# Performance work log

Hardware: AMD Instinct MI355X
Metric: run time of the kernel (lower is better)

## Reference

```python
import jax, jax.numpy as jnp
import numpy as np
from jax import lax

IMG = 512
STRIDE = 32
FH = IMG // STRIDE  # 16
TOP_N = 1000
NCLS = 6  # num_classes + background
BBOX_CLAMP = float(np.log(1000.0 / 16.0))


def _conv(x, w, b, stride, pad):
    y = lax.conv_general_dilated(x, w, (stride, stride), [(pad, pad), (pad, pad)],
                                 dimension_numbers=('NCHW', 'OIHW', 'NCHW'))
    return y + b[None, :, None, None]


def _decode(deltas, boxes, weights):
    # torchvision BoxCoder.decode_single; deltas (N,K,4), boxes (N,4) xyxy
    wx, wy, ww, wh = weights
    widths = boxes[:, 2] - boxes[:, 0]
    heights = boxes[:, 3] - boxes[:, 1]
    cx = boxes[:, 0] + 0.5 * widths
    cy = boxes[:, 1] + 0.5 * heights
    dx = deltas[..., 0] / wx
    dy = deltas[..., 1] / wy
    dw = jnp.minimum(deltas[..., 2] / ww, BBOX_CLAMP)
    dh = jnp.minimum(deltas[..., 3] / wh, BBOX_CLAMP)
    pcx = dx * widths[:, None] + cx[:, None]
    pcy = dy * heights[:, None] + cy[:, None]
    pw = jnp.exp(dw) * widths[:, None]
    ph = jnp.exp(dh) * heights[:, None]
    return jnp.stack([pcx - 0.5 * pw, pcy - 0.5 * ph,
                      pcx + 0.5 * pw, pcy + 0.5 * ph], axis=-1)


def _anchors():
    # AnchorGenerator(sizes=(128,256,512), ratios=(0.5,1,2)), single stride-32 level
    scales = np.array([128.0, 256.0, 512.0])
    ratios = np.array([0.5, 1.0, 2.0])
    h_r = np.sqrt(ratios)
    w_r = 1.0 / h_r
    ws = (w_r[:, None] * scales[None, :]).reshape(-1)
    hs = (h_r[:, None] * scales[None, :]).reshape(-1)
    cell = np.round(np.stack([-ws, -hs, ws, hs], axis=1) / 2.0)  # (9,4)
    sy, sx = np.meshgrid(np.arange(FH) * STRIDE, np.arange(FH) * STRIDE, indexing='ij')
    shifts = np.stack([sx.reshape(-1), sy.reshape(-1), sx.reshape(-1), sy.reshape(-1)], axis=1)
    anc = (shifts[:, None, :] + cell[None, :, :]).reshape(-1, 4)  # (FH*FH*9, 4), (h,w,A) order
    return jnp.asarray(anc, jnp.float32)


def _roi_align(feat_nhwc, rois, bidx):
    # torchvision roi_align: output 7x7, sampling_ratio=2, spatial_scale=1/32, aligned=False
    scale = 1.0 / STRIDE
    Wf = feat_nhwc.shape[1]
    x1 = rois[:, 0] * scale
    y1 = rois[:, 1] * scale
    x2 = rois[:, 2] * scale
    y2 = rois[:, 3] * scale
    rw = jnp.maximum(x2 - x1, 1.0)
    rh = jnp.maximum(y2 - y1, 1.0)
    # 14 = 7 bins * 2 samples; point k sits at (k+0.5)*bin/2 from roi start
    g = (jnp.arange(14, dtype=jnp.float32) + 0.5) / 14.0
    px = jnp.clip(x1[:, None] + g[None, :] * rw[:, None], 0.0, Wf - 1)  # (R,14)
    py = jnp.clip(y1[:, None] + g[None, :] * rh[:, None], 0.0, Wf - 1)
    x0 = jnp.floor(px).astype(jnp.int32)
    y0 = jnp.floor(py).astype(jnp.int32)
    x1i = jnp.minimum(x0 + 1, Wf - 1)
    y1i = jnp.minimum(y0 + 1, Wf - 1)
    lx = px - x0.astype(px.dtype)
    ly = py - y0.astype(py.dtype)
    hx = 1.0 - lx
    hy = 1.0 - ly
    b = bidx[:, None, None]

    def gat(yi, xi):
        return feat_nhwc[b, yi[:, :, None], xi[:, None, :]]  # (R,14,14,C)

    ly_ = ly[:, :, None, None]; hy_ = hy[:, :, None, None]
    lx_ = lx[:, None, :, None]; hx_ = hx[:, None, :, None]
    s = (hy_ * hx_ * gat(y0, x0) + hy_ * lx_ * gat(y0, x1i)
         + ly_ * hx_ * gat(y1i, x0) + ly_ * lx_ * gat(y1i, x1i))  # (R,14,14,C)
    R, C = s.shape[0], s.shape[3]
    pooled = s.reshape(R, 7, 2, 7, 2, C).mean(axis=(2, 4))  # (R,7,7,C)
    return pooled.transpose(0, 3, 1, 2).reshape(R, C * 49)


def _forward(images, c0_w, c0_b, c1_w, c1_b, c2_w, c2_b, c3_w, c3_b,
             rpn_conv_w, rpn_conv_b, rpn_cls_w, rpn_cls_b, rpn_bbox_w, rpn_bbox_b,
             fc1_w, fc1_b, fc2_w, fc2_b, cls_w, cls_b, bbox_w, bbox_b):
    B = images.shape[0]
    # GeneralizedRCNNTransform: normalize; resize is identity (512 == min_size)
    mean = jnp.array([0.485, 0.456, 0.406], jnp.float32).reshape(1, 3, 1, 1)
    std = jnp.array([0.229, 0.224, 0.225], jnp.float32).reshape(1, 3, 1, 1)
    x = (images - mean) / std
    # backbone: stride-32, 512-channel feature extractor (resnet34-style features_only)
    x = jax.nn.relu(_conv(x, c0_w, c0_b, 2, 3))
    x = lax.reduce_window(x, -jnp.inf, lax.max, (1, 1, 3, 3), (1, 1, 2, 2),
                          [(0, 0), (0, 0), (1, 1), (1, 1)])
    x = jax.nn.relu(_conv(x, c1_w, c1_b, 2, 1))
    x = jax.nn.relu(_conv(x, c2_w, c2_b, 2, 1))
    feat = jax.nn.relu(_conv(x, c3_w, c3_b, 2, 1))  # (B,512,16,16)
    # RPN head
    t = jax.nn.relu(_conv(feat, rpn_conv_w, rpn_conv_b, 1, 1))
    obj = _conv(t, rpn_cls_w, rpn_cls_b, 1, 0)   # (B,9,16,16)
    bd = _conv(t, rpn_bbox_w, rpn_bbox_b, 1, 0)  # (B,36,16,16)
    _, A, H, W = obj.shape
    # concat_box_prediction_layers ordering: (H,W,A)
    obj_f = lax.stop_gradient(obj.transpose(0, 2, 3, 1).reshape(B, -1))  # (B,N)
    bd_f = lax.stop_gradient(
        bd.reshape(B, A, 4, H, W).transpose(0, 3, 4, 1, 2).reshape(B, -1, 4))  # (B,N,4)
    anchors = _anchors()  # (N,4)
    props = _decode(bd_f.transpose(1, 0, 2), anchors, (1.0, 1.0, 1.0, 1.0)).transpose(1, 0, 2)
    # _get_top_n_idx (single level, eval pre_nms_top_n=1000) + gather + clip
    _, top_idx = lax.top_k(obj_f, TOP_N)
    props = props[jnp.arange(B)[:, None], top_idx]  # (B,TOP_N,4)
    props = jnp.clip(props, 0.0, float(IMG))
    rois = props.reshape(-1, 4)
    bidx = jnp.repeat(jnp.arange(B), TOP_N)
    # MultiScaleRoIAlign -> TwoMLPHead -> FastRCNNPredictor
    bf = _roi_align(feat.transpose(0, 2, 3, 1), rois, bidx)  # (R, 512*49)
    h = jax.nn.relu(bf @ fc1_w + fc1_b)
    h = jax.nn.relu(h @ fc2_w + fc2_b)
    logits = h @ cls_w + cls_b  # (R,6)
    breg = h @ bbox_w + bbox_b  # (R,24)
    pred = _decode(breg.reshape(-1, NCLS, 4), rois, (10.0, 10.0, 5.0, 5.0))  # (R,6,4)
    scores = jax.nn.softmax(logits, axis=1)[:, 1:]   # drop background -> (R,5)
    boxes = jnp.clip(pred, 0.0, float(IMG))[:, 1:]   # (R,5,4)
    # resize ratios original/transformed = 512/512 = 1.0 -> coordinate rescale is identity
    out = jnp.concatenate([boxes, scores[:, :, None]], axis=2)  # (R,5,5)
    return out.reshape(B, -1, NCLS - 1, 5)  # (B,1000,5,5)


_SHAPES = {
    'c0_w': (64, 3, 7, 7), 'c0_b': (64,),
    'c1_w': (128, 64, 3, 3), 'c1_b': (128,),
    'c2_w': (256, 128, 3, 3), 'c2_b': (256,),
    'c3_w': (512, 256, 3, 3), 'c3_b': (512,),
    'rpn_conv_w': (512, 512, 3, 3), 'rpn_conv_b': (512,),
    'rpn_cls_w': (9, 512, 1, 1), 'rpn_cls_b': (9,),
    'rpn_bbox_w': (36, 512, 1, 1), 'rpn_bbox_b': (36,),
    'fc1_w': (25088, 1024), 'fc1_b': (1024,),
    'fc2_w': (1024, 1024), 'fc2_b': (1024,),
    'cls_w': (1024, 6), 'cls_b': (6,),
    'bbox_w': (1024, 24), 'bbox_b': (24,),
}


def setup_inputs() -> dict:
    key = jax.random.key(0)
    ks = jax.random.split(key, len(_SHAPES) + 1)
    inp = {'images': jax.random.normal(ks[0], (1, 3, IMG, IMG), jnp.float32)}
    for i, (name, shp) in enumerate(_SHAPES.items()):
        if name.endswith('_b'):
            inp[name] = jnp.zeros(shp, jnp.float32)
        else:
            fan_in = int(np.prod(shp[1:])) if len(shp) == 4 else int(shp[0])
            scale = float(np.sqrt(2.0 / fan_in))
            if name in ('rpn_bbox_w', 'bbox_w'):
                scale *= 0.1  # keep box deltas small/realistic
            inp[name] = jax.random.normal(ks[i + 1], shp, jnp.float32) * scale
    return inp


def reference(images, c0_w, c0_b, c1_w, c1_b, c2_w, c2_b, c3_w, c3_b,
              rpn_conv_w, rpn_conv_b, rpn_cls_w, rpn_cls_b, rpn_bbox_w, rpn_bbox_b,
              fc1_w, fc1_b, fc2_w, fc2_b, cls_w, cls_b, bbox_w, bbox_b):
    return _forward(images, c0_w, c0_b, c1_w, c1_b, c2_w, c2_b, c3_w, c3_b,
                    rpn_conv_w, rpn_conv_b, rpn_cls_w, rpn_cls_b, rpn_bbox_w, rpn_bbox_b,
                    fc1_w, fc1_b, fc2_w, fc2_b, cls_w, cls_b, bbox_w, bbox_b)
```

## Files before the change

kernel.cpp:

```cpp
#include <hip/hip_runtime.h>
#include <cstdint>
#include <cstddef>


typedef float  f4  __attribute__((ext_vector_type(4)));
typedef short  s8v __attribute__((ext_vector_type(8)));

__device__ __forceinline__ unsigned short f2bf(float f) {
  unsigned int u = __builtin_bit_cast(unsigned int, f);
  u += 0x7FFFu + ((u >> 16) & 1u);
  return (unsigned short)(u >> 16);
}
__device__ __forceinline__ float bf2f(unsigned short h) {
  unsigned int u = ((unsigned int)h) << 16;
  return __builtin_bit_cast(float, u);
}

#define BBOX_CLAMP_F 4.135166556742356f

__global__ __launch_bounds__(256, 2) void conv0_kernel(
    const float* __restrict__ img, const float* __restrict__ w,
    const float* __restrict__ bias, float* __restrict__ out) {
  __shared__ float patch[3][37][40];
  __shared__ float wlds[32][3][7][8];
  const int tid = threadIdx.x;
  const int tx0 = blockIdx.x * 16, ty0 = blockIdx.y * 16;
  const int ocb = blockIdx.z * 32;
  for (int idx = tid; idx < 3 * 37 * 40; idx += 256) {
    int c = idx / 1480; int rem = idx - c * 1480; int r = rem / 40; int col = rem - r * 40;
    float v = 0.f;
    int iy = ty0 * 2 - 3 + r, ix = tx0 * 2 - 3 + col;
    if (col < 37 && iy >= 0 && iy < 512 && ix >= 0 && ix < 512) {
      float mval = (c == 0) ? 0.485f : (c == 1) ? 0.456f : 0.406f;
      float sval = (c == 0) ? 0.229f : (c == 1) ? 0.224f : 0.225f;
      v = (img[c * 262144 + iy * 512 + ix] - mval) / sval;
    }
    (&patch[0][0][0])[idx] = v;
  }
  for (int idx = tid; idx < 32 * 3 * 7 * 8; idx += 256) {
    int oc = idx / 168; int rem = idx - oc * 168; int c = rem / 56;
    int rem2 = rem - c * 56; int ky = rem2 >> 3; int kx = rem2 & 7;
    (&wlds[0][0][0][0])[idx] = (kx < 7) ? w[(ocb + oc) * 147 + c * 49 + ky * 7 + kx] : 0.f;
  }
  __syncthreads();
  const int ocg = tid >> 5, cell = tid & 31;
  const int cx = cell & 3, cy = cell >> 2;
  float acc[4][2][4] = {};
  for (int c = 0; c < 3; ++c) {
    for (int ky = 0; ky < 7; ++ky) {
      const float* p0 = &patch[c][cy * 4 + ky][cx * 8];
      const float* p1 = &patch[c][cy * 4 + ky + 2][cx * 8];
      f4 a0[4], a1[4];
      #pragma unroll
      for (int q = 0; q < 4; ++q) { a0[q] = *(const f4*)(p0 + q * 4); a1[q] = *(const f4*)(p1 + q * 4); }
      #pragma unroll
      for (int oc = 0; oc < 4; ++oc) {
        const float* wp = &wlds[ocg * 4 + oc][c][ky][0];
        f4 w0 = *(const f4*)wp, w1 = *(const f4*)(wp + 4);
        #pragma unroll
        for (int kx = 0; kx < 7; ++kx) {
          float wv = (kx < 4) ? w0[kx] : w1[kx - 4];
          #pragma unroll
          for (int x = 0; x < 4; ++x) {
            int e = x * 2 + kx;
            acc[oc][0][x] += a0[e >> 2][e & 3] * wv;
            acc[oc][1][x] += a1[e >> 2][e & 3] * wv;
          }
        }
      }
    }
  }
  #pragma unroll
  for (int oc = 0; oc < 4; ++oc) {
    float b = bias[ocb + ocg * 4 + oc];
    #pragma unroll
    for (int r = 0; r < 2; ++r) {
      f4 v;
      #pragma unroll
      for (int x = 0; x < 4; ++x) v[x] = fmaxf(acc[oc][r][x] + b, 0.f);
      *(f4*)&out[(size_t)(ocb + ocg * 4 + oc) * 65536 + (size_t)(ty0 + cy * 2 + r) * 256 + tx0 + cx * 4] = v;
    }
  }
}

__global__ __launch_bounds__(256) void maxpool_kernel(
    const float* __restrict__ in, float* __restrict__ out) {
  int i = blockIdx.x * 256 + threadIdx.x;
  int c = i >> 14; int y = (i >> 7) & 127; int x = i & 127;
  float m = -INFINITY;
  #pragma unroll
  for (int dy = 0; dy < 3; ++dy) {
    int yy = 2 * y - 1 + dy;
    if (yy < 0 || yy >= 256) continue;
    #pragma unroll
    for (int dx = 0; dx < 3; ++dx) {
      int xx = 2 * x - 1 + dx;
      if (xx < 0 || xx >= 256) continue;
      m = fmaxf(m, in[c * 65536 + yy * 256 + xx]);
    }
  }
  out[i] = m;
}

template<int CIN, int COUT, int HIN, int HOUT, int STR, int TILES_X, int CSPL>
__global__ __launch_bounds__(256, 2) void conv3x3_kernel(
    const float* __restrict__ in, const float* __restrict__ w,
    float* __restrict__ parts) {
  constexpr int TW = 16, TH = 16;
  constexpr int SPAN  = (TH - 1) * STR + 3;
  constexpr int SPANW = (TW - 1) * STR + 3;
  constexpr int PADW  = (SPANW + 3) & ~3;
  __shared__ float patch[8][SPAN][PADW];
  __shared__ float wlds[32][8][3][4];
  const int tid = threadIdx.x;
  const int tile = blockIdx.x;
  const int tx0 = (tile % TILES_X) * TW, ty0 = (tile / TILES_X) * TH;
  const int ocb = blockIdx.y * 32;
  const int cb0 = blockIdx.z * CSPL;
  const int ocg = tid >> 5, cell = tid & 31;
  const int cx = cell & 3, cy = cell >> 2;
  float acc[4][2][4] = {};
  for (int cc = 0; cc < CSPL / 8; ++cc) {
    int cbase = cb0 + cc * 8;
    __syncthreads();
    for (int idx = tid; idx < 8 * SPAN * PADW; idx += 256) {
      int ch = idx / (SPAN * PADW);
      int rem = idx - ch * (SPAN * PADW);
      int r = rem / PADW;
      int col = rem - r * PADW;
      float v = 0.f;
      int iy = ty0 * STR - 1 + r, ix = tx0 * STR - 1 + col;
      if (col < SPANW && iy >= 0 && iy < HIN && ix >= 0 && ix < HIN)
        v = in[(size_t)(cbase + ch) * (HIN * HIN) + iy * HIN + ix];
      (&patch[0][0][0])[idx] = v;
    }
    for (int idx = tid; idx < 32 * 8 * 3 * 4; idx += 256) {
      int oc = idx / 96;
      int rem = idx - oc * 96;
      int ch = rem / 12;
      int rem2 = rem - ch * 12;
      int ky = rem2 >> 2, kx = rem2 & 3;
      (&wlds[0][0][0][0])[idx] = (kx < 3)
        ? w[((size_t)(ocb + oc) * CIN + cbase + ch) * 9 + ky * 3 + kx] : 0.f;
    }
    __syncthreads();
    #pragma unroll 1
    for (int ch = 0; ch < 8; ++ch) {
      #pragma unroll
      for (int ky = 0; ky < 3; ++ky) {
        constexpr int NF = (STR == 2) ? 3 : 2;
        const float* p0 = &patch[ch][(cy * 2 + 0) * STR + ky][cx * 4 * STR];
        const float* p1 = &patch[ch][(cy * 2 + 1) * STR + ky][cx * 4 * STR];
        f4 a0[NF], a1[NF];
        #pragma unroll
        for (int q = 0; q < NF; ++q) { a0[q] = *(const f4*)(p0 + q * 4); a1[q] = *(const f4*)(p1 + q * 4); }
        #pragma unroll
        for (int oc = 0; oc < 4; ++oc) {
          f4 wv = *(const f4*)&wlds[ocg * 4 + oc][ch][ky][0];
          #pragma unroll
          for (int kx = 0; kx < 3; ++kx) {
            #pragma unroll
            for (int x = 0; x < 4; ++x) {
              int e = x * STR + kx;
              acc[oc][0][x] += a0[e >> 2][e & 3] * wv[kx];
              acc[oc][1][x] += a1[e >> 2][e & 3] * wv[kx];
            }
          }
        }
      }
    }
  }
  size_t zb = (size_t)blockIdx.z * COUT * HOUT * HOUT;
  #pragma unroll
  for (int oc = 0; oc < 4; ++oc) {
    #pragma unroll
    for (int r = 0; r < 2; ++r) {
      f4 v;
      #pragma unroll
      for (int x = 0; x < 4; ++x) v[x] = acc[oc][r][x];
      *(f4*)&parts[zb + (size_t)(ocb + ocg * 4 + oc) * (HOUT * HOUT)
                   + (size_t)(ty0 + cy * 2 + r) * HOUT + tx0 + cx * 4] = v;
    }
  }
}

template<int NS>
__global__ __launch_bounds__(256) void reduce_conv_kernel(
    const float* __restrict__ parts, const float* __restrict__ bias,
    float* __restrict__ out, int total4, int hwshift,
    unsigned short* __restrict__ nhwc, float* __restrict__ nhwc32, int C) {
  int i4 = blockIdx.x * 256 + threadIdx.x;
  if (i4 >= total4) return;
  const f4* p4 = (const f4*)parts;
  f4 s = {0.f, 0.f, 0.f, 0.f};
  #pragma unroll
  for (int k = 0; k < NS; ++k) s += p4[(size_t)k * total4 + i4];
  int i = i4 * 4;
  int c = i >> hwshift;
  float b = bias[c];
  #pragma unroll
  for (int j = 0; j < 4; ++j) s[j] = fmaxf(s[j] + b, 0.f);
  ((f4*)out)[i4] = s;
  int hw = 1 << hwshift;
  int px = i & (hw - 1);
  if (nhwc) {
    #pragma unroll
    for (int j = 0; j < 4; ++j) nhwc[(size_t)(px + j) * C + c] = f2bf(s[j]);
  }
  if (nhwc32) {
    #pragma unroll
    for (int j = 0; j < 4; ++j) nhwc32[(size_t)(px + j) * C + c] = s[j];
  }
}

__global__ __launch_bounds__(64) void rpn_head_kernel(
    const float* __restrict__ tn, const float* __restrict__ wc,
    const float* __restrict__ bc, const float* __restrict__ wb,
    const float* __restrict__ bb, float* __restrict__ objf,
    float* __restrict__ bdf) {
  int px = blockIdx.x, lane = threadIdx.x;
  float acc[45] = {};
  for (int j = 0; j < 8; ++j) {
    int c = j * 64 + lane;
    float tv = tn[px * 512 + c];
    #pragma unroll
    for (int a = 0; a < 9; ++a) acc[a] += tv * wc[a * 512 + c];
    #pragma unroll
    for (int o = 0; o < 36; ++o) acc[9 + o] += tv * wb[o * 512 + c];
  }
  #pragma unroll
  for (int o = 0; o < 45; ++o) {
    #pragma unroll
    for (int m = 32; m; m >>= 1) acc[o] += __shfl_xor(acc[o], m);
  }
  if (lane == 0) {
    #pragma unroll
    for (int a = 0; a < 9; ++a) objf[px * 9 + a] = acc[a] + bc[a];
    #pragma unroll
    for (int a = 0; a < 9; ++a)
      #pragma unroll
      for (int q = 0; q < 4; ++q)
        bdf[(px * 9 + a) * 4 + q] = acc[9 + a * 4 + q] + bb[a * 4 + q];
  }
}

__device__ const float g_W2[9] = {91.f, 181.f, 362.f, 64.f, 128.f, 256.f, 45.f, 91.f, 181.f};
__device__ const float g_H2[9] = {45.f, 91.f, 181.f, 64.f, 128.f, 256.f, 91.f, 181.f, 362.f};

__global__ __launch_bounds__(256) void props_kernel(
    const float* __restrict__ bdf, float* __restrict__ props) {
  int i = blockIdx.x * 256 + threadIdx.x;
  if (i >= 2304) return;
  int pix = i / 9; int a = i - pix * 9;
  int y = pix >> 4, x = pix & 15;
  float wid = 2.f * g_W2[a], hei = 2.f * g_H2[a];
  float cx = (float)(x * 32), cy = (float)(y * 32);
  float dx = bdf[i * 4 + 0], dy = bdf[i * 4 + 1];
  float dw = fminf(bdf[i * 4 + 2], BBOX_CLAMP_F);
  float dh = fminf(bdf[i * 4 + 3], BBOX_CLAMP_F);
  float pcx = dx * wid + cx, pcy = dy * hei + cy;
  float pw = expf(dw) * wid, ph = expf(dh) * hei;
  props[i * 4 + 0] = fminf(fmaxf(pcx - 0.5f * pw, 0.f), 512.f);
  props[i * 4 + 1] = fminf(fmaxf(pcy - 0.5f * ph, 0.f), 512.f);
  props[i * 4 + 2] = fminf(fmaxf(pcx + 0.5f * pw, 0.f), 512.f);
  props[i * 4 + 3] = fminf(fmaxf(pcy + 0.5f * ph, 0.f), 512.f);
}

__global__ __launch_bounds__(256) void topk_kernel(
    const float* __restrict__ objf, const float* __restrict__ props,
    float* __restrict__ rois) {
  __shared__ float v[2304];
  int tid = threadIdx.x;
  for (int idx = tid; idx < 2304; idx += 256) v[idx] = objf[idx];
  __syncthreads();
  int i = blockIdx.x * 256 + tid;
  float vi = v[i];
  int rank = 0;
  for (int j = 0; j < 2304; ++j) {
    float vj = v[j];
    rank += (vj > vi) || (vj == vi && j < i);
  }
  if (rank < 1000) {
    f4 p = *(const f4*)(props + i * 4);
    *(f4*)(rois + rank * 4) = p;
  }
}

__global__ __launch_bounds__(256) void roi_align_kernel(
    const float* __restrict__ rois, const unsigned short* __restrict__ featn,
    unsigned short* __restrict__ A) {
  __shared__ int   pidx[49][16];
  __shared__ float pwg[49][16];
  int m = blockIdx.x, tid = threadIdx.x;
  if (tid < 49) {
    int qy = tid / 7, qx = tid - qy * 7;
    float x1 = rois[m * 4 + 0] * 0.03125f;
    float y1 = rois[m * 4 + 1] * 0.03125f;
    float x2 = rois[m * 4 + 2] * 0.03125f;
    float y2 = rois[m * 4 + 3] * 0.03125f;
    float rw = fmaxf(x2 - x1, 1.f), rh = fmaxf(y2 - y1, 1.f);
    float wsx[2][2]; int xsx[2][2];
    float wsy[2][2]; int ysy[2][2];
    #pragma unroll
    for (int s = 0; s < 2; ++s) {
      float gx = ((float)(2 * qx + s) + 0.5f) / 14.f;
      float px = fminf(fmaxf(x1 + gx * rw, 0.f), 15.f);
      int x0 = (int)floorf(px);
      int x1i = min(x0 + 1, 15);
      float lx = px - (float)x0;
      xsx[s][0] = x0; xsx[s][1] = x1i; wsx[s][0] = 1.f - lx; wsx[s][1] = lx;
      float gy = ((float)(2 * qy + s) + 0.5f) / 14.f;
      float py = fminf(fmaxf(y1 + gy * rh, 0.f), 15.f);
      int y0 = (int)floorf(py);
      int y1i = min(y0 + 1, 15);
      float ly = py - (float)y0;
      ysy[s][0] = y0; ysy[s][1] = y1i; wsy[s][0] = 1.f - ly; wsy[s][1] = ly;
    }
    int e = 0;
    #pragma unroll
    for (int sy = 0; sy < 2; ++sy)
      #pragma unroll
      for (int cyi = 0; cyi < 2; ++cyi)
        #pragma unroll
        for (int sx = 0; sx < 2; ++sx)
          #pragma unroll
          for (int cxi = 0; cxi < 2; ++cxi) {
            pwg[tid][e] = 0.25f * wsy[sy][cyi] * wsx[sx][cxi];
            pidx[tid][e] = (ysy[sy][cyi] * 16 + xsx[sx][cxi]) * 256;
            ++e;
          }
  }
  __syncthreads();
  const unsigned int* F2 = (const unsigned int*)featn;
  unsigned int* A2 = (unsigned int*)A;
  size_t base = (size_t)m * 12544 + tid;
  for (int p = 0; p < 49; ++p) {
    float a0 = 0.f, a1 = 0.f;
    #pragma unroll
    for (int e = 0; e < 16; ++e) {
      unsigned int u = F2[pidx[p][e] + tid];
      float wgt = pwg[p][e];
      a0 += wgt * bf2f((unsigned short)(u & 0xffffu));
      a1 += wgt * bf2f((unsigned short)(u >> 16));
    }
    A2[base + (size_t)p * 256] =
        (unsigned int)f2bf(a0) | ((unsigned int)f2bf(a1) << 16);
  }
}

__global__ __launch_bounds__(256) void transpose_fc1_kernel(
    const float* __restrict__ src, unsigned short* __restrict__ dst) {
  __shared__ float tile[64][65];
  int p = blockIdx.x;
  int c0 = blockIdx.y * 64;
  int n0 = blockIdx.z * 64;
  int tid = threadIdx.x;
  int rr = tid >> 4, c4 = tid & 15;
  #pragma unroll
  for (int j = 0; j < 4; ++j) {
    int c = rr + j * 16;
    f4 v = *(const f4*)(src + (size_t)((c0 + c) * 49 + p) * 1024 + n0 + c4 * 4);
    tile[c][c4 * 4 + 0] = v[0]; tile[c][c4 * 4 + 1] = v[1];
    tile[c][c4 * 4 + 2] = v[2]; tile[c][c4 * 4 + 3] = v[3];
  }
  __syncthreads();
  int nl = tid >> 2;
  int kc = (tid & 3) * 16;
  unsigned int u[8];
  #pragma unroll
  for (int i = 0; i < 8; ++i) {
    unsigned int lo = f2bf(tile[kc + 2 * i][nl]);
    unsigned int hi = f2bf(tile[kc + 2 * i + 1][nl]);
    u[i] = lo | (hi << 16);
  }
  uint4* dp = (uint4*)(dst + (size_t)(n0 + nl) * 25088 + p * 512 + c0 + kc);
  dp[0] = make_uint4(u[0], u[1], u[2], u[3]);
  dp[1] = make_uint4(u[4], u[5], u[6], u[7]);
}

__global__ __launch_bounds__(256) void transpose_bf16_kernel(
    const float* __restrict__ src, unsigned short* __restrict__ dst,
    int K, int N) {
  __shared__ float tile[64][65];
  int k0 = blockIdx.x * 64, n0 = blockIdx.y * 64;
  int tid = threadIdx.x;
  int rr = tid >> 4, c4 = tid & 15;
  #pragma unroll
  for (int j = 0; j < 4; ++j) {
    int r = rr + j * 16;
    f4 v = *(const f4*)(src + (size_t)(k0 + r) * N + n0 + c4 * 4);
    tile[r][c4 * 4 + 0] = v[0]; tile[r][c4 * 4 + 1] = v[1];
    tile[r][c4 * 4 + 2] = v[2]; tile[r][c4 * 4 + 3] = v[3];
  }
  __syncthreads();
  int nl = tid >> 2;
  int kc = (tid & 3) * 16;
  unsigned int u[8];
  #pragma unroll
  for (int i = 0; i < 8; ++i) {
    unsigned int lo = f2bf(tile[kc + 2 * i][nl]);
    unsigned int hi = f2bf(tile[kc + 2 * i + 1][nl]);
    u[i] = lo | (hi << 16);
  }
  uint4* dp = (uint4*)(dst + (size_t)(n0 + nl) * K + k0 + kc);
  dp[0] = make_uint4(u[0], u[1], u[2], u[3]);
  dp[1] = make_uint4(u[4], u[5], u[6], u[7]);
}

__global__ __launch_bounds__(256, 2) void gemm_bt_kernel(
    const unsigned short* __restrict__ A, const unsigned short* __restrict__ B,
    float* __restrict__ parts, int K, int nsteps) {
  __shared__ unsigned short As[128 * 32];
  __shared__ unsigned short Bs[128 * 32];
  const int tid = threadIdx.x;
  const int lane = tid & 63, wave = tid >> 6;
  const int n0 = blockIdx.x * 128, m0 = blockIdx.y * 128, ks = blockIdx.z;
  const int kbase = ks * nsteps * 32;
  f4 acc[4][4] = {};
  const int wr = wave >> 1, wc = wave & 1;
  const int rsel = lane & 15, ksel = (lane >> 4) * 8;
  for (int s = 0; s < nsteps; ++s) {
    int kk = kbase + s * 32;
    #pragma unroll
    for (int j = 0; j < 2; ++j) {
      int c_ = j * 256 + tid;
      int row = c_ >> 2;
      int k8 = (c_ & 3) << 3;
      __builtin_amdgcn_global_load_lds(
          (const __attribute__((address_space(1))) void*)(A + (size_t)(m0 + row) * K + kk + k8),
          (__attribute__((address_space(3))) void*)(As + c_ * 8), 16, 0, 0);
      __builtin_amdgcn_global_load_lds(
          (const __attribute__((address_space(1))) void*)(B + (size_t)(n0 + row) * K + kk + k8),
          (__attribute__((address_space(3))) void*)(Bs + c_ * 8), 16, 0, 0);
    }
    __syncthreads();
    s8v af[4], bfr[4];
    #pragma unroll
    for (int m = 0; m < 4; ++m)
      af[m] = *(const s8v*)(As + (wr * 64 + m * 16 + rsel) * 32 + ksel);
    #pragma unroll
    for (int n = 0; n < 4; ++n)
      bfr[n] = *(const s8v*)(Bs + (wc * 64 + n * 16 + rsel) * 32 + ksel);
    #pragma unroll
    for (int m = 0; m < 4; ++m)
      #pragma unroll
      for (int n = 0; n < 4; ++n)
        acc[m][n] = __builtin_amdgcn_mfma_f32_16x16x32_bf16(af[m], bfr[n], acc[m][n], 0, 0, 0);
    __syncthreads();
  }
  float* outp = parts + (size_t)ks * 1048576;
  int rb = m0 + wr * 64 + ((lane >> 4) << 2);
  int cb = n0 + wc * 64 + (lane & 15);
  #pragma unroll
  for (int m = 0; m < 4; ++m)
    #pragma unroll
    for (int n = 0; n < 4; ++n)
      #pragma unroll
      for (int i = 0; i < 4; ++i)
        outp[(size_t)(rb + m * 16 + i) * 1024 + cb + n * 16] = acc[m][n][i];
}

__global__ __launch_bounds__(256) void reduce_fc1_kernel(
    const float* __restrict__ parts, const float* __restrict__ bias,
    unsigned short* __restrict__ h1b) {
  int i4 = blockIdx.x * 256 + threadIdx.x;
  const f4* p4 = (const f4*)parts;
  f4 s = {0.f, 0.f, 0.f, 0.f};
  #pragma unroll
  for (int k = 0; k < 8; ++k) s += p4[(size_t)k * 262144 + i4];
  f4 b = ((const f4*)bias)[i4 & 255];
  s += b;
  unsigned int lo = (unsigned int)f2bf(fmaxf(s[0], 0.f)) | ((unsigned int)f2bf(fmaxf(s[1], 0.f)) << 16);
  unsigned int hi = (unsigned int)f2bf(fmaxf(s[2], 0.f)) | ((unsigned int)f2bf(fmaxf(s[3], 0.f)) << 16);
  ((uint2*)h1b)[i4] = make_uint2(lo, hi);
}

__global__ __launch_bounds__(256) void reduce_fc2_kernel(
    const float* __restrict__ parts, const float* __restrict__ bias,
    float* __restrict__ h2) {
  int i4 = blockIdx.x * 256 + threadIdx.x;
  const f4* p4 = (const f4*)parts;
  f4 s = p4[i4] + p4[262144 + i4];
  f4 b = ((const f4*)bias)[i4 & 255];
  s += b;
  #pragma unroll
  for (int j = 0; j < 4; ++j) s[j] = fmaxf(s[j], 0.f);
  ((f4*)h2)[i4] = s;
}

__global__ __launch_bounds__(256) void heads_kernel(
    const float* __restrict__ h2, const float* __restrict__ cw,
    const float* __restrict__ cb, const float* __restrict__ bw,
    const float* __restrict__ bb, const float* __restrict__ rois,
    float* __restrict__ outp) {
  int m = blockIdx.x, tid = threadIdx.x;
  int lane = tid & 63, wv = tid >> 6;
  __shared__ float vals[32];
  const float* hrow = h2 + (size_t)m * 1024;
  float acc[8] = {};
  for (int k = lane; k < 1024; k += 64) {
    float hv = hrow[k];
    #pragma unroll
    for (int j = 0; j < 8; ++j) {
      int o = wv * 8 + j;
      float wval = 0.f;
      if (o < 6) wval = cw[k * 6 + o];
      else if (o < 30) wval = bw[k * 24 + o - 6];
      acc[j] += hv * wval;
    }
  }
  #pragma unroll
  for (int j = 0; j < 8; ++j) {
    #pragma unroll
    for (int s = 32; s; s >>= 1) acc[j] += __shfl_xor(acc[j], s);
  }
  if (lane == 0) {
    #pragma unroll
    for (int j = 0; j < 8; ++j) {
      int o = wv * 8 + j;
      if (o < 6) vals[o] = acc[j] + cb[o];
      else if (o < 30) vals[o] = acc[j] + bb[o - 6];
    }
  }
  __syncthreads();
  if (tid < 5) {
    int cls = tid + 1;
    float mx = vals[0];
    #pragma unroll
    for (int o = 1; o < 6; ++o) mx = fmaxf(mx, vals[o]);
    float den = 0.f;
    #pragma unroll
    for (int o = 0; o < 6; ++o) den += expf(vals[o] - mx);
    float score = expf(vals[cls] - mx) / den;
    float x1 = rois[m * 4 + 0], y1 = rois[m * 4 + 1];
    float x2 = rois[m * 4 + 2], y2 = rois[m * 4 + 3];
    float w_ = x2 - x1, h_ = y2 - y1;
    float cxx = x1 + 0.5f * w_, cyy = y1 + 0.5f * h_;
    float dx = vals[6 + cls * 4 + 0] / 10.f;
    float dy = vals[6 + cls * 4 + 1] / 10.f;
    float dw = fminf(vals[6 + cls * 4 + 2] / 5.f, BBOX_CLAMP_F);
    float dh = fminf(vals[6 + cls * 4 + 3] / 5.f, BBOX_CLAMP_F);
    float pcx = dx * w_ + cxx, pcy = dy * h_ + cyy;
    float pw = expf(dw) * w_, ph = expf(dh) * h_;
    float* op = outp + m * 25 + tid * 5;
    op[0] = fminf(fmaxf(pcx - 0.5f * pw, 0.f), 512.f);
    op[1] = fminf(fmaxf(pcy - 0.5f * ph, 0.f), 512.f);
    op[2] = fminf(fmaxf(pcx + 0.5f * pw, 0.f), 512.f);
    op[3] = fminf(fmaxf(pcy + 0.5f * ph, 0.f), 512.f);
    op[4] = score;
  }
}

static constexpr size_t MB_ = 1024ull * 1024ull;
static constexpr size_t A_OFF      = 0;
static constexpr size_t CONV0_OFF  = 0;
static constexpr size_t POOL_OFF   = 17 * MB_;
static constexpr size_t C1_OFF     = 22 * MB_;
static constexpr size_t C2_OFF     = 25 * MB_;
static constexpr size_t CPARTS_OFF = 27 * MB_;
static constexpr size_t FEAT_OFF   = 52 * MB_;
static constexpr size_t FEATN_OFF  = FEAT_OFF + 524288;
static constexpr size_t T_OFF      = FEATN_OFF + 262144;
static constexpr size_t OBJF_OFF   = T_OFF + 524288;
static constexpr size_t BDF_OFF    = OBJF_OFF + 16384;
static constexpr size_t PROPS_OFF  = BDF_OFF + 40960;
static constexpr size_t ROIS_OFF   = PROPS_OFF + 40960;
static constexpr size_t TN_OFF     = ROIS_OFF + 16384;
static constexpr size_t BT1_OFF    = 54 * MB_;
static constexpr size_t H1B_OFF    = BT1_OFF;
static constexpr size_t BT2_OFF    = BT1_OFF + 2 * MB_;
static constexpr size_t PARTS2_OFF = BT1_OFF + 4 * MB_;
static constexpr size_t H2_OFF     = BT1_OFF + 13 * MB_;
static constexpr size_t PARTS1_OFF = 106 * MB_;

extern "C" void kernel_launch(void* const* d_in, const int* in_sizes, int n_in,
                              void* d_out, int out_size, void* d_ws, size_t ws_size,
                              hipStream_t stream) {
  (void)in_sizes; (void)n_in; (void)out_size; (void)ws_size;
  const float* images     = (const float*)d_in[0];
  const float* c0_w       = (const float*)d_in[1];
  const float* c0_b       = (const float*)d_in[2];
  const float* c1_w       = (const float*)d_in[3];
  const float* c1_b       = (const float*)d_in[4];
  const float* c2_w       = (const float*)d_in[5];
  const float* c2_b       = (const float*)d_in[6];
  const float* c3_w       = (const float*)d_in[7];
  const float* c3_b       = (const float*)d_in[8];
  const float* rpn_conv_w = (const float*)d_in[9];
  const float* rpn_conv_b = (const float*)d_in[10];
  const float* rpn_cls_w  = (const float*)d_in[11];
  const float* rpn_cls_b  = (const float*)d_in[12];
  const float* rpn_bbox_w = (const float*)d_in[13];
  const float* rpn_bbox_b = (const float*)d_in[14];
  const float* fc1_w      = (const float*)d_in[15];
  const float* fc1_b      = (const float*)d_in[16];
  const float* fc2_w      = (const float*)d_in[17];
  const float* fc2_b      = (const float*)d_in[18];
  const float* cls_w      = (const float*)d_in[19];
  const float* cls_b      = (const float*)d_in[20];
  const float* bbox_w     = (const float*)d_in[21];
  const float* bbox_b     = (const float*)d_in[22];

  char* ws = (char*)d_ws;
  float* conv0  = (float*)(ws + CONV0_OFF);
  float* pool   = (float*)(ws + POOL_OFF);
  float* c1o    = (float*)(ws + C1_OFF);
  float* c2o    = (float*)(ws + C2_OFF);
  float* cparts = (float*)(ws + CPARTS_OFF);
  float* feat   = (float*)(ws + FEAT_OFF);
  unsigned short* featn = (unsigned short*)(ws + FEATN_OFF);
  float* tbuf   = (float*)(ws + T_OFF);
  float* objf   = (float*)(ws + OBJF_OFF);
  float* bdf    = (float*)(ws + BDF_OFF);
  float* props  = (float*)(ws + PROPS_OFF);
  float* rois   = (float*)(ws + ROIS_OFF);
  float* tn     = (float*)(ws + TN_OFF);
  unsigned short* Abuf = (unsigned short*)(ws + A_OFF);
  unsigned short* Bt1  = (unsigned short*)(ws + BT1_OFF);
  unsigned short* h1b  = (unsigned short*)(ws + H1B_OFF);
  unsigned short* Bt2  = (unsigned short*)(ws + BT2_OFF);
  float* parts1 = (float*)(ws + PARTS1_OFF);
  float* parts2 = (float*)(ws + PARTS2_OFF);
  float* h2     = (float*)(ws + H2_OFF);
  float* outp   = (float*)d_out;

  conv0_kernel<<<dim3(16, 16, 2), 256, 0, stream>>>(images, c0_w, c0_b, conv0);
  maxpool_kernel<<<4096, 256, 0, stream>>>(conv0, pool);
  conv3x3_kernel<64, 128, 128, 64, 2, 4, 8><<<dim3(16, 4, 8), 256, 0, stream>>>(pool, c1_w, cparts);
  reduce_conv_kernel<8><<<512, 256, 0, stream>>>(cparts, c1_b, c1o, 131072, 12, nullptr, nullptr, 0);
  conv3x3_kernel<128, 256, 64, 32, 2, 2, 8><<<dim3(4, 8, 16), 256, 0, stream>>>(c1o, c2_w, cparts);
  reduce_conv_kernel<16><<<256, 256, 0, stream>>>(cparts, c2_b, c2o, 65536, 10, nullptr, nullptr, 0);
  conv3x3_kernel<256, 512, 32, 16, 2, 1, 8><<<dim3(1, 16, 32), 256, 0, stream>>>(c2o, c3_w, cparts);
  reduce_conv_kernel<32><<<128, 256, 0, stream>>>(cparts, c3_b, feat, 32768, 8, featn, nullptr, 512);

  conv3x3_kernel<512, 512, 16, 16, 1, 1, 16><<<dim3(1, 16, 32), 256, 0, stream>>>(feat, rpn_conv_w, cparts);
  reduce_conv_kernel<32><<<128, 256, 0, stream>>>(cparts, rpn_conv_b, tbuf, 32768, 8, nullptr, tn, 512);
  rpn_head_kernel<<<256, 64, 0, stream>>>(tn, rpn_cls_w, rpn_cls_b, rpn_bbox_w, rpn_bbox_b, objf, bdf);
  props_kernel<<<9, 256, 0, stream>>>(bdf, props);
  topk_kernel<<<9, 256, 0, stream>>>(objf, props, rois);

  hipMemsetAsync(ws + A_OFF + (size_t)1000 * 25088 * 2, 0, (size_t)24 * 25088 * 2, stream);
  roi_align_kernel<<<1000, 256, 0, stream>>>(rois, featn, Abuf);

  transpose_fc1_kernel<<<dim3(49, 8, 16), 256, 0, stream>>>(fc1_w, Bt1);
  gemm_bt_kernel<<<dim3(8, 8, 8), 256, 0, stream>>>(Abuf, Bt1, parts1, 25088, 98);
  reduce_fc1_kernel<<<1024, 256, 0, stream>>>(parts1, fc1_b, h1b);

  transpose_bf16_kernel<<<dim3(16, 16), 256, 0, stream>>>(fc2_w, Bt2, 1024, 1024);
  gemm_bt_kernel<<<dim3(8, 8, 2), 256, 0, stream>>>(h1b, Bt2, parts2, 1024, 16);
  reduce_fc2_kernel<<<1024, 256, 0, stream>>>(parts2, fc2_b, h2);

  heads_kernel<<<1000, 256, 0, stream>>>(h2, cls_w, cls_b, bbox_w, bbox_b, rois, outp);
}
```

Before: 704.8 us.

## Double fc1 split-K, store bf16 partials, widen roi_align channel loads

The fc1 GEMM's split-K factor goes from 8 to 16, giving 1024 blocks instead of 512 for better CU occupancy, and launch bounds are raised to 4 blocks per CU. The partial sums are now written in bf16 rather than fp32, which keeps the partial-buffer traffic about the same despite twice as many slices. The reduction kernel sums 16 bf16 slices. RoI-align now handles 4 channels per thread with 8-byte loads, with two sampling points processed in parallel across half-blocks. Rounding each partial to bf16 before reduction adds precision loss to the fc1 accumulation.

```diff
diff --git a/kernel.cpp b/kernel.cpp
--- a/kernel.cpp
+++ b/kernel.cpp
@@ -326,25 +326,34 @@
           #pragma unroll
           for (int cxi = 0; cxi < 2; ++cxi) {
             pwg[tid][e] = 0.25f * wsy[sy][cyi] * wsx[sx][cxi];
-            pidx[tid][e] = (ysy[sy][cyi] * 16 + xsx[sx][cxi]) * 256;
+            pidx[tid][e] = (ysy[sy][cyi] * 16 + xsx[sx][cxi]) * 128;
             ++e;
           }
   }
   __syncthreads();
-  const unsigned int* F2 = (const unsigned int*)featn;
-  unsigned int* A2 = (unsigned int*)A;
-  size_t base = (size_t)m * 12544 + tid;
-  for (int p = 0; p < 49; ++p) {
-    float a0 = 0.f, a1 = 0.f;
-    #pragma unroll
-    for (int e = 0; e < 16; ++e) {
-      unsigned int u = F2[pidx[p][e] + tid];
-      float wgt = pwg[p][e];
-      a0 += wgt * bf2f((unsigned short)(u & 0xffffu));
-      a1 += wgt * bf2f((unsigned short)(u >> 16));
-    }
-    A2[base + (size_t)p * 256] =
-        (unsigned int)f2bf(a0) | ((unsigned int)f2bf(a1) << 16);
+  const uint2* F4 = (const uint2*)featn;
+  uint2* A4 = (uint2*)A;
+  int cpair = tid & 127;
+  int psel  = tid >> 7;
+  size_t base = (size_t)m * 6272 + cpair;
+  for (int p0 = 0; p0 < 49; p0 += 2) {
+    int p = p0 + psel;
+    if (p < 49) {
+      float a0 = 0.f, a1 = 0.f, a2 = 0.f, a3 = 0.f;
+      #pragma unroll
+      for (int e = 0; e < 16; ++e) {
+        uint2 u = F4[pidx[p][e] + cpair];
+        float wgt = pwg[p][e];
+        a0 += wgt * bf2f((unsigned short)(u.x & 0xffffu));
+        a1 += wgt * bf2f((unsigned short)(u.x >> 16));
+        a2 += wgt * bf2f((unsigned short)(u.y & 0xffffu));
+        a3 += wgt * bf2f((unsigned short)(u.y >> 16));
+      }
+      uint2 o;
+      o.x = (unsigned int)f2bf(a0) | ((unsigned int)f2bf(a1) << 16);
+      o.y = (unsigned int)f2bf(a2) | ((unsigned int)f2bf(a3) << 16);
+      A4[base + (size_t)p * 128] = o;
+    }
   }
 }
 
@@ -407,9 +416,10 @@
   dp[1] = make_uint4(u[4], u[5], u[6], u[7]);
 }
 
-__global__ __launch_bounds__(256, 2) void gemm_bt_kernel(
+template<bool BF16P>
+__global__ __launch_bounds__(256, 4) void gemm_bt_kernel(
     const unsigned short* __restrict__ A, const unsigned short* __restrict__ B,
-    float* __restrict__ parts, int K, int nsteps) {
+    void* __restrict__ parts, int K, int nsteps) {
   __shared__ unsigned short As[128 * 32];
   __shared__ unsigned short Bs[128 * 32];
   const int tid = threadIdx.x;
@@ -448,31 +458,48 @@
         acc[m][n] = __builtin_amdgcn_mfma_f32_16x16x32_bf16(af[m], bfr[n], acc[m][n], 0, 0, 0);
     __syncthreads();
   }
-  float* outp = parts + (size_t)ks * 1048576;
   int rb = m0 + wr * 64 + ((lane >> 4) << 2);
   int cb = n0 + wc * 64 + (lane & 15);
-  #pragma unroll
-  for (int m = 0; m < 4; ++m)
-    #pragma unroll
-    for (int n = 0; n < 4; ++n)
-      #pragma unroll
-      for (int i = 0; i < 4; ++i)
-        outp[(size_t)(rb + m * 16 + i) * 1024 + cb + n * 16] = acc[m][n][i];
+  if constexpr (BF16P) {
+    unsigned short* outp = (unsigned short*)parts + (size_t)ks * 1048576;
+    #pragma unroll
+    for (int m = 0; m < 4; ++m)
+      #pragma unroll
+      for (int n = 0; n < 4; ++n)
+        #pragma unroll
+        for (int i = 0; i < 4; ++i)
+          outp[(size_t)(rb + m * 16 + i) * 1024 + cb + n * 16] = f2bf(acc[m][n][i]);
+  } else {
+    float* outp = (float*)parts + (size_t)ks * 1048576;
+    #pragma unroll
+    for (int m = 0; m < 4; ++m)
+      #pragma unroll
+      for (int n = 0; n < 4; ++n)
+        #pragma unroll
+        for (int i = 0; i < 4; ++i)
+          outp[(size_t)(rb + m * 16 + i) * 1024 + cb + n * 16] = acc[m][n][i];
+  }
 }
 
 __global__ __launch_bounds__(256) void reduce_fc1_kernel(
-    const float* __restrict__ parts, const float* __restrict__ bias,
+    const unsigned short* __restrict__ parts, const float* __restrict__ bias,
     unsigned short* __restrict__ h1b) {
-  int i4 = blockIdx.x * 256 + threadIdx.x;
-  const f4* p4 = (const f4*)parts;
-  f4 s = {0.f, 0.f, 0.f, 0.f};
-  #pragma unroll
-  for (int k = 0; k < 8; ++k) s += p4[(size_t)k * 262144 + i4];
-  f4 b = ((const f4*)bias)[i4 & 255];
-  s += b;
-  unsigned int lo = (unsigned int)f2bf(fmaxf(s[0], 0.f)) | ((unsigned int)f2bf(fmaxf(s[1], 0.f)) << 16);
-  unsigned int hi = (unsigned int)f2bf(fmaxf(s[2], 0.f)) | ((unsigned int)f2bf(fmaxf(s[3], 0.f)) << 16);
-  ((uint2*)h1b)[i4] = make_uint2(lo, hi);
+  int i2 = blockIdx.x * 256 + threadIdx.x;
+  const uint2* p2 = (const uint2*)parts;
+  float s0 = 0.f, s1 = 0.f, s2 = 0.f, s3 = 0.f;
+  #pragma unroll
+  for (int k = 0; k < 16; ++k) {
+    uint2 u = p2[(size_t)k * 262144 + i2];
+    s0 += bf2f((unsigned short)(u.x & 0xffffu));
+    s1 += bf2f((unsigned short)(u.x >> 16));
+    s2 += bf2f((unsigned short)(u.y & 0xffffu));
+    s3 += bf2f((unsigned short)(u.y >> 16));
+  }
+  f4 b = ((const f4*)bias)[i2 & 255];
+  s0 += b[0]; s1 += b[1]; s2 += b[2]; s3 += b[3];
+  unsigned int lo = (unsigned int)f2bf(fmaxf(s0, 0.f)) | ((unsigned int)f2bf(fmaxf(s1, 0.f)) << 16);
+  unsigned int hi = (unsigned int)f2bf(fmaxf(s2, 0.f)) | ((unsigned int)f2bf(fmaxf(s3, 0.f)) << 16);
+  ((uint2*)h1b)[i2] = make_uint2(lo, hi);
 }
 
 __global__ __launch_bounds__(256) void reduce_fc2_kernel(
@@ -619,7 +646,7 @@
   unsigned short* Bt1  = (unsigned short*)(ws + BT1_OFF);
   unsigned short* h1b  = (unsigned short*)(ws + H1B_OFF);
   unsigned short* Bt2  = (unsigned short*)(ws + BT2_OFF);
-  float* parts1 = (float*)(ws + PARTS1_OFF);
+  unsigned short* parts1b = (unsigned short*)(ws + PARTS1_OFF);
   float* parts2 = (float*)(ws + PARTS2_OFF);
   float* h2     = (float*)(ws + H2_OFF);
   float* outp   = (float*)d_out;
@@ -643,11 +670,11 @@
   roi_align_kernel<<<1000, 256, 0, stream>>>(rois, featn, Abuf);
 
   transpose_fc1_kernel<<<dim3(49, 8, 16), 256, 0, stream>>>(fc1_w, Bt1);
-  gemm_bt_kernel<<<dim3(8, 8, 8), 256, 0, stream>>>(Abuf, Bt1, parts1, 25088, 98);
-  reduce_fc1_kernel<<<1024, 256, 0, stream>>>(parts1, fc1_b, h1b);
+  gemm_bt_kernel<true><<<dim3(8, 8, 16), 256, 0, stream>>>(Abuf, Bt1, parts1b, 25088, 49);
+  reduce_fc1_kernel<<<1024, 256, 0, stream>>>(parts1b, fc1_b, h1b);
 
   transpose_bf16_kernel<<<dim3(16, 16), 256, 0, stream>>>(fc2_w, Bt2, 1024, 1024);
-  gemm_bt_kernel<<<dim3(8, 8, 2), 256, 0, stream>>>(h1b, Bt2, parts2, 1024, 16);
+  gemm_bt_kernel<false><<<dim3(8, 8, 2), 256, 0, stream>>>(h1b, Bt2, parts2, 1024, 16);
   reduce_fc2_kernel<<<1024, 256, 0, stream>>>(parts2, fc2_b, h2);
 
   heads_kernel<<<1000, 256, 0, stream>>>(h2, cls_w, cls_b, bbox_w, bbox_b, rois, outp);
```

New measurement: 691.7 us. About the same (-1.9%).
